# Kernel tuning notes

Hardware: AMD Instinct MI355X
Metric: run time of the kernel (lower is better)

## Reference

```python
import jax, jax.numpy as jnp
import numpy as np

N, E, B, H, L = 100000, 200000, 2048, 256, 4
EPS_MSG = 1e-7   # GENConv message eps
LN_EPS = 1e-5    # torch LayerNorm default eps
SM_EPS = 1e-16   # PyG softmax denominator eps


def layer_norm(x, g, b):
    mu = x.mean(-1, keepdims=True)
    var = ((x - mu) ** 2).mean(-1, keepdims=True)
    return (x - mu) * jax.lax.rsqrt(var + LN_EPS) * g + b


def gen_conv(x, src, dst, eattr, t, W1, b1, lg, lb, W2, b2):
    # GENConv(aggr='softmax', learn_t, num_layers=2, norm='layer')
    msg = jax.nn.relu(x[src] + eattr) + EPS_MSG                      # [E,H]
    scaled = msg * t
    seg_max = jax.ops.segment_max(scaled, dst, num_segments=N)       # [N,H]
    seg_max = jnp.where(jnp.isfinite(seg_max), seg_max, 0.0)
    ex = jnp.exp(scaled - seg_max[dst])                              # [E,H]
    denom = jax.ops.segment_sum(ex, dst, num_segments=N)             # [N,H]
    alpha = ex / (denom[dst] + SM_EPS)
    out = jax.ops.segment_sum(msg * alpha, dst, num_segments=N)      # [N,H]
    out = out + x                                                    # root residual inside GENConv
    h = jax.nn.relu(layer_norm(out @ W1 + b1, lg, lb))               # MLP: Lin -> LN -> ReLU -> Lin
    return h @ W2 + b2


def setup_inputs() -> dict:
    key = jax.random.key(0)
    ks = iter(jax.random.split(key, 16))
    s = lambda *sh: jax.random.normal(next(ks), sh, jnp.float32) * 0.05
    return dict(
        x=jax.random.normal(next(ks), (N, 9), jnp.float32),
        edge_index=jax.random.randint(next(ks), (2, E), 0, N),
        edge_attr=jax.random.normal(next(ks), (E, 3), jnp.float32),
        batch=jnp.sort(jax.random.randint(next(ks), (N,), 0, B)),
        node_W=s(9, H), node_b=jnp.zeros((H,), jnp.float32),
        edge_W=s(3, H), edge_b=jnp.zeros((H,), jnp.float32),
        vn_emb=jnp.zeros((1, H), jnp.float32),
        ln_g=jnp.ones((L, H), jnp.float32), ln_b=jnp.zeros((L, H), jnp.float32),
        t=jnp.ones((L - 1,), jnp.float32),
        mlp_W1=s(L - 1, H, 2 * H), mlp_b1=jnp.zeros((L - 1, 2 * H), jnp.float32),
        mlp_ln_g=jnp.ones((L - 1, 2 * H), jnp.float32), mlp_ln_b=jnp.zeros((L - 1, 2 * H), jnp.float32),
        mlp_W2=s(L - 1, 2 * H, H), mlp_b2=jnp.zeros((L - 1, H), jnp.float32),
    )


def reference(x, edge_index, edge_attr, batch, node_W, node_b, edge_W, edge_b,
              vn_emb, ln_g, ln_b, t, mlp_W1, mlp_b1, mlp_ln_g, mlp_ln_b, mlp_W2, mlp_b2):
    src, dst = edge_index[0], edge_index[1]
    h = x @ node_W + node_b                                          # node encoder
    ea = edge_attr @ edge_W + edge_b                                 # edge encoder
    vn = jnp.broadcast_to(vn_emb, (B, H))
    counts = jax.ops.segment_sum(jnp.ones((N,), h.dtype), batch, num_segments=B)
    inv_counts = (1.0 / jnp.maximum(counts, 1.0))[:, None]           # [B,1]
    # layers[1:] run conv (block='res+'); layers[0] supplies only the final norm+act
    for l in range(1, L):
        hn = jax.nn.relu(layer_norm(h, ln_g[l], ln_b[l]))            # dropout=0.1 is a no-op in eval
        h = h + gen_conv(hn, src, dst, ea, t[l - 1],
                         mlp_W1[l - 1], mlp_b1[l - 1], mlp_ln_g[l - 1], mlp_ln_b[l - 1],
                         mlp_W2[l - 1], mlp_b2[l - 1])
        vn = vn + jax.ops.segment_sum(h, batch, num_segments=B) * inv_counts  # scatter_mean
        h = h + vn[batch]                                            # broadcast virtual node
    h = jax.nn.relu(layer_norm(h, ln_g[0], ln_b[0]))
    return jax.ops.segment_sum(h, batch, num_segments=B) * inv_counts  # global_mean_pool [B,H]
```

## Files before the change

### kernel.cpp

```cpp
#include <hip/hip_runtime.h>
#include <cstdint>
#include <cstddef>


typedef _Float16 half8_t __attribute__((ext_vector_type(8)));
typedef _Float16 half4_t __attribute__((ext_vector_type(4)));
typedef float    floatx4 __attribute__((ext_vector_type(4)));

#define DEVINL __device__ __forceinline__

DEVINL float wave_sum(float v) {
#pragma unroll
  for (int m = 32; m; m >>= 1) v += __shfl_xor(v, m, 64);
  return v;
}

__global__ __launch_bounds__(256) void k_node_enc(
    const float* __restrict__ x, const float* __restrict__ W,
    const float* __restrict__ bias, _Float16* __restrict__ h, int Nr) {
  __shared__ float sW[9 * 256];
  __shared__ float sb[256];
  __shared__ float sx[72];
  const int j = threadIdx.x;
#pragma unroll
  for (int k = 0; k < 9; ++k) sW[k * 256 + j] = W[k * 256 + j];
  sb[j] = bias[j];
  const int row0 = blockIdx.x * 8;
  if (j < 72) {
    int p = row0 * 9 + j;
    sx[j] = (p < Nr * 9) ? x[p] : 0.f;
  }
  __syncthreads();
  for (int r = 0; r < 8; ++r) {
    int row = row0 + r;
    if (row >= Nr) break;
    float acc = sb[j];
#pragma unroll
    for (int k = 0; k < 9; ++k) acc = fmaf(sx[r * 9 + k], sW[k * 256 + j], acc);
    h[(size_t)row * 256 + j] = (_Float16)acc;
  }
}

__global__ void k_bptr(const int* __restrict__ batch, int* __restrict__ bptr,
                       int N_, int B_) {
  int b = blockIdx.x * 256 + threadIdx.x;
  if (b > B_) return;
  int lo = 0, hi = N_;
  while (lo < hi) {
    int mid = (lo + hi) >> 1;
    if (batch[mid] < b) lo = mid + 1; else hi = mid;
  }
  bptr[b] = lo;
}

__global__ void k_deg(const int* __restrict__ ei, int* __restrict__ deg, int E_) {
  int e = blockIdx.x * 256 + threadIdx.x;
  if (e < E_) atomicAdd(&deg[ei[E_ + e]], 1);
}

__global__ __launch_bounds__(256) void k_scan1(
    const int* __restrict__ in, int* __restrict__ out1, int* __restrict__ bsum, int n) {
  __shared__ int tmp[256];
  const int t = threadIdx.x;
  const int base = blockIdx.x * 1024;
  int v[4];
  int run = 0;
#pragma unroll
  for (int i = 0; i < 4; ++i) {
    int p = base + t * 4 + i;
    int xv = (p < n) ? in[p] : 0;
    run += xv;
    v[i] = run;
  }
  tmp[t] = run;
  __syncthreads();
  for (int off = 1; off < 256; off <<= 1) {
    int u = (t >= off) ? tmp[t - off] : 0;
    __syncthreads();
    tmp[t] += u;
    __syncthreads();
  }
  int excl = tmp[t] - run;
#pragma unroll
  for (int i = 0; i < 4; ++i) {
    int p = base + t * 4 + i;
    if (p < n) out1[p] = v[i] + excl;
  }
  if (t == 255) bsum[blockIdx.x] = tmp[255];
}

__global__ void k_scan2(int* bsum, int nb, int* ptr0) {
  if (threadIdx.x == 0 && blockIdx.x == 0) {
    int run = 0;
    for (int i = 0; i < nb; ++i) { int xv = bsum[i]; bsum[i] = run; run += xv; }
    ptr0[0] = 0;
  }
}

__global__ __launch_bounds__(256) void k_scan3(int* out1, const int* __restrict__ bsum, int n) {
  int add = bsum[blockIdx.x];
  int p0 = blockIdx.x * 1024 + threadIdx.x * 4;
#pragma unroll
  for (int i = 0; i < 4; ++i) {
    int p = p0 + i;
    if (p < n) out1[p] += add;
  }
}

__global__ void k_copy(const int* __restrict__ a, int* __restrict__ b, int n) {
  int i = blockIdx.x * 256 + threadIdx.x;
  if (i < n) b[i] = a[i];
}

__global__ void k_csrfill(const int* __restrict__ ei, int* __restrict__ cursor,
                          int* __restrict__ csr_src, int* __restrict__ csr_eid, int E_) {
  int e = blockIdx.x * 256 + threadIdx.x;
  if (e < E_) {
    int d = ei[E_ + e];
    int pos = atomicAdd(&cursor[d], 1);
    csr_src[pos] = ei[e];
    csr_eid[pos] = e;
  }
}

__global__ void k_vninit(const float* __restrict__ emb, float* __restrict__ vn) {
  vn[(size_t)blockIdx.x * 256 + threadIdx.x] = emb[threadIdx.x];
}

__global__ __launch_bounds__(256) void k_wcvt_all(
    const float* __restrict__ W1, const float* __restrict__ W2,
    _Float16* __restrict__ W1T, _Float16* __restrict__ W2T) {
  int idx = blockIdx.x * 256 + threadIdx.x;
  int mat = idx >> 17;
  int rem = idx & 131071;
  if (mat < 3) {
    int k = rem >> 9, n = rem & 511;
    W1T[(size_t)mat * 131072 + (size_t)n * 256 + k] =
        (_Float16)W1[(size_t)mat * 131072 + rem];
  } else {
    int m = mat - 3;
    int k = rem >> 8, n = rem & 255;
    W2T[(size_t)m * 131072 + (size_t)n * 512 + k] =
        (_Float16)W2[(size_t)m * 131072 + rem];
  }
}

__global__ __launch_bounds__(256) void k_ln256(
    const _Float16* __restrict__ h, const float* __restrict__ g,
    const float* __restrict__ b, _Float16* __restrict__ out, int Nr) {
  int row = blockIdx.x * 4 + (threadIdx.x >> 6);
  if (row >= Nr) return;
  int lane = threadIdx.x & 63;
  half4_t xh = *(const half4_t*)(h + (size_t)row * 256 + lane * 4);
  float x0 = (float)xh[0], x1 = (float)xh[1], x2 = (float)xh[2], x3 = (float)xh[3];
  float s = wave_sum(x0 + x1 + x2 + x3);
  float mu = s * (1.f / 256.f);
  float d0 = x0 - mu, d1 = x1 - mu, d2 = x2 - mu, d3 = x3 - mu;
  float v = wave_sum(d0 * d0 + d1 * d1 + d2 * d2 + d3 * d3);
  float rstd = rsqrtf(v * (1.f / 256.f) + 1e-5f);
  float4 gv = *(const float4*)(g + lane * 4);
  float4 bv = *(const float4*)(b + lane * 4);
  half4_t o;
  o[0] = (_Float16)fmaxf(d0 * rstd * gv.x + bv.x, 0.f);
  o[1] = (_Float16)fmaxf(d1 * rstd * gv.y + bv.y, 0.f);
  o[2] = (_Float16)fmaxf(d2 * rstd * gv.z + bv.z, 0.f);
  o[3] = (_Float16)fmaxf(d3 * rstd * gv.w + bv.w, 0.f);
  *(half4_t*)(out + (size_t)row * 256 + lane * 4) = o;
}

__global__ __launch_bounds__(256) void k_aggregate(
    const _Float16* __restrict__ hn, const float* __restrict__ eattr,
    const float* __restrict__ edgeW, const float* __restrict__ edgeB,
    const int* __restrict__ indptr, const int* __restrict__ csr_src,
    const int* __restrict__ csr_eid, const float* __restrict__ tptr,
    _Float16* __restrict__ agg, int Nr) {
  int node = blockIdx.x * 4 + (threadIdx.x >> 6);
  if (node >= Nr) return;
  int lane = threadIdx.x & 63;
  int j0 = lane * 4;
  float4 w0 = *(const float4*)(edgeW + j0);
  float4 w1 = *(const float4*)(edgeW + 256 + j0);
  float4 w2 = *(const float4*)(edgeW + 512 + j0);
  float4 wb = *(const float4*)(edgeB + j0);
  float W0[4] = {w0.x, w0.y, w0.z, w0.w};
  float W1r[4] = {w1.x, w1.y, w1.z, w1.w};
  float W2r[4] = {w2.x, w2.y, w2.z, w2.w};
  float WB[4] = {wb.x, wb.y, wb.z, wb.w};
  float tval = tptr[0];
  int e0 = indptr[node], e1 = indptr[node + 1];
  float D[4] = {0.f, 0.f, 0.f, 0.f};
  float Nu[4] = {0.f, 0.f, 0.f, 0.f};
  for (int s = e0; s < e1; ++s) {
    int srcn = csr_src[s];
    int eid = csr_eid[s];
    float ex0 = eattr[(size_t)eid * 3 + 0];
    float ex1 = eattr[(size_t)eid * 3 + 1];
    float ex2 = eattr[(size_t)eid * 3 + 2];
    half4_t hv = *(const half4_t*)(hn + (size_t)srcn * 256 + j0);
#pragma unroll
    for (int i = 0; i < 4; ++i) {
      float eaj = fmaf(ex0, W0[i], fmaf(ex1, W1r[i], fmaf(ex2, W2r[i], WB[i])));
      float msg = fmaxf((float)hv[i] + eaj, 0.f) + 1e-7f;
      float pr = __expf(msg * tval);
      D[i] += pr;
      Nu[i] = fmaf(pr, msg, Nu[i]);
    }
  }
  half4_t hs = *(const half4_t*)(hn + (size_t)node * 256 + j0);
  half4_t res;
#pragma unroll
  for (int i = 0; i < 4; ++i)
    res[i] = (_Float16)(Nu[i] / (D[i] + 1e-16f) + (float)hs[i]);
  *(half4_t*)(agg + (size_t)node * 256 + j0) = res;
}

__global__ __launch_bounds__(256, 3) void k_gemm1(
    const _Float16* __restrict__ A, const _Float16* __restrict__ BT,
    const float* __restrict__ bias, _Float16* __restrict__ outh,
    float2* __restrict__ rstat, int M) {
  __shared__ _Float16 ldsA[64 * 256];
  __shared__ _Float16 ldsB[128 * 64];
  const int tid = threadIdx.x;
  const int lane = tid & 63;
  const int wv = tid >> 6;
  const int m0 = blockIdx.x * 64;
  const int wm = wv * 16;
  const int q = lane >> 4;
  const int l16 = lane & 15;

  {
    half8_t tmp[8];
    int ss[8];
#pragma unroll
    for (int g = 0; g < 8; ++g) {
      int s = g * 256 + tid;
      int r = s >> 5;
      int c = (s & 31) ^ (r & 7);
      int rowA = m0 + r;
      rowA = rowA < M ? rowA : (M - 1);
      tmp[g] = *(const half8_t*)(A + (size_t)rowA * 256 + c * 8);
      ss[g] = s;
    }
#pragma unroll
    for (int g = 0; g < 8; ++g)
      *(half8_t*)(ldsA + (size_t)ss[g] * 8) = tmp[g];
  }

  size_t offB[4];
  int ldsOffB[4];
#pragma unroll
  for (int i = 0; i < 4; ++i) {
    int p = (i * 4 + wv) * 64 + lane;
    int r = p >> 3;
    int s = p & 7;
    int gg = s ^ (r & 7);
    offB[i] = (size_t)r * 256 + gg * 8;
    ldsOffB[i] = p * 8;
  }
  half8_t rb[4];
  auto loadB = [&](int j) {
    int n = j >> 2, t = j & 3;
    size_t base = (size_t)n * 128 * 256 + t * 64;
#pragma unroll
    for (int i = 0; i < 4; ++i)
      rb[i] = *(const half8_t*)(BT + base + offB[i]);
  };
  auto writeB = [&]() {
#pragma unroll
    for (int i = 0; i < 4; ++i)
      *(half8_t*)(ldsB + ldsOffB[i]) = rb[i];
  };

  floatx4 acc[8] = {};
  float sA[4] = {0.f, 0.f, 0.f, 0.f}, s2A[4] = {0.f, 0.f, 0.f, 0.f};

  loadB(0);
  writeB();
  for (int j = 0; j < 16; ++j) {
    __syncthreads();
    if (j + 1 < 16) loadB(j + 1);
    const int t = j & 3;
#pragma unroll
    for (int kk = 0; kk < 2; ++kk) {
      const int c8 = kk * 4 + q;
      const int cg = t * 8 + c8;
      int r = wm + l16;
      half8_t af = *(const half8_t*)(ldsA + (size_t)(r * 32 + (cg ^ (r & 7))) * 8);
      half8_t bf[8];
#pragma unroll
      for (int ct = 0; ct < 8; ++ct) {
        int n = ct * 16 + l16;
        bf[ct] = *(const half8_t*)(ldsB + (size_t)(n * 8 + (c8 ^ (n & 7))) * 8);
      }
#pragma unroll
      for (int ct = 0; ct < 8; ++ct)
        acc[ct] = __builtin_amdgcn_mfma_f32_16x16x32_f16(af, bf[ct], acc[ct], 0, 0, 0);
    }
    __syncthreads();
    if (j + 1 < 16) writeB();
    if ((j & 3) == 3) {
      int n = j >> 2;
#pragma unroll
      for (int rr = 0; rr < 4; ++rr) {
        int row = m0 + wm + q * 4 + rr;
        float vv[8];
        float s = 0.f, s2 = 0.f;
#pragma unroll
        for (int ct = 0; ct < 8; ++ct) {
          int col = n * 128 + ct * 16 + l16;
          float v = acc[ct][rr] + bias[col];
          vv[ct] = v;
          s += v;
          s2 += v * v;
        }
        if (row < M) {
#pragma unroll
          for (int ct = 0; ct < 8; ++ct) {
            int col = n * 128 + ct * 16 + l16;
            outh[(size_t)row * 512 + col] = (_Float16)vv[ct];
          }
        }
        sA[rr] += s;
        s2A[rr] += s2;
      }
#pragma unroll
      for (int ct = 0; ct < 8; ++ct)
        acc[ct] = floatx4{0.f, 0.f, 0.f, 0.f};
    }
  }

#pragma unroll
  for (int rr = 0; rr < 4; ++rr) {
    float s = sA[rr], s2 = s2A[rr];
#pragma unroll
    for (int m = 1; m < 16; m <<= 1) {
      s += __shfl_xor(s, m, 64);
      s2 += __shfl_xor(s2, m, 64);
    }
    int row = m0 + wm + q * 4 + rr;
    if (l16 == 0 && row < M) rstat[row] = make_float2(s, s2);
  }
}

template <int VN>
__global__ __launch_bounds__(256, 2) void k_gemm2(
    const _Float16* __restrict__ A, const _Float16* __restrict__ BT,
    const float* __restrict__ bias, const float2* __restrict__ rstat,
    const float* __restrict__ lg, const float* __restrict__ lb,
    const float* __restrict__ vn, const int* __restrict__ batch,
    _Float16* __restrict__ outf, int M) {
  constexpr int K = 512, NN = 256, NT = K / 64;
  constexpr int EPS = 68;
  const int g = blockIdx.x;
  const int mI = blockIdx.y * 8 + (g & 7);
  const int nI = g >> 3;
  const int mT = (M + 127) >> 7;
  if (mI >= mT) return;

  __shared__ _Float16 ldsbuf[4 * 64 * EPS];
  _Float16* ldsA = ldsbuf;
  _Float16* ldsB = ldsbuf + 128 * 64;
  __shared__ float sg[512];
  __shared__ float sbt[512];
  const int tid = threadIdx.x;
  sg[tid] = lg[tid];
  sg[tid + 256] = lg[tid + 256];
  sbt[tid] = lb[tid];
  sbt[tid + 256] = lb[tid + 256];
  __syncthreads();

  const int lane = tid & 63;
  const int wv = tid >> 6;
  const int m0 = mI * 128;
  const int n0 = nI * 128;
  const int wm = (wv >> 1) * 64;
  const int wn = (wv & 1) * 64;
  const int q = lane >> 4;
  const int l16 = lane & 15;
  floatx4 acc[4][4] = {};

  size_t offA[4], offB[4];
  int ldsOff[4], gcolA[4];
  float aco[4], cco[4];
#pragma unroll
  for (int i = 0; i < 4; ++i) {
    int p = (i * 4 + wv) * 64 + lane;
    int r = p >> 3;
    int s = p & 7;
    int gg = s ^ (r & 7);
    int rowA = m0 + r;
    rowA = rowA < M ? rowA : (M - 1);
    offA[i] = (size_t)rowA * K + gg * 8;
    offB[i] = (size_t)(n0 + r) * K + gg * 8;
    ldsOff[i] = p * 8;
    gcolA[i] = gg * 8;
    float2 st = rstat[rowA];
    float mu = st.x * (1.f / 512.f);
    float var = st.y * (1.f / 512.f) - mu * mu;
    float rs = rsqrtf(var + 1e-5f);
    aco[i] = rs;
    cco[i] = -mu * rs;
  }
  half8_t ra[4], rb[4];
  auto loadtile = [&](int kt) {
#pragma unroll
    for (int i = 0; i < 4; ++i) {
      ra[i] = *(const half8_t*)(A + offA[i] + kt);
      rb[i] = *(const half8_t*)(BT + offB[i] + kt);
    }
  };
  auto writetile = [&](int kt) {
#pragma unroll
    for (int i = 0; i < 4; ++i) {
      int c0 = kt + gcolA[i];
      half8_t ya;
#pragma unroll
      for (int jj = 0; jj < 8; ++jj) {
        float e = fmaf((float)ra[i][jj], aco[i], cco[i]);
        float y = fmaf(e, sg[c0 + jj], sbt[c0 + jj]);
        ya[jj] = (_Float16)fmaxf(y, 0.f);
      }
      *(half8_t*)(ldsA + ldsOff[i]) = ya;
      *(half8_t*)(ldsB + ldsOff[i]) = rb[i];
    }
  };

  loadtile(0);
  writetile(0);
#pragma unroll
  for (int t = 0; t < NT; ++t) {
    __syncthreads();
    if (t + 1 < NT) loadtile((t + 1) * 64);
#pragma unroll
    for (int kk = 0; kk < 2; ++kk) {
      half8_t af[4], bf[4];
      const int c8 = kk * 4 + q;
#pragma unroll
      for (int rt = 0; rt < 4; ++rt) {
        int r = wm + rt * 16 + l16;
        af[rt] = *(const half8_t*)(ldsA + (size_t)(r * 8 + (c8 ^ (r & 7))) * 8);
      }
#pragma unroll
      for (int ct = 0; ct < 4; ++ct) {
        int n = wn + ct * 16 + l16;
        bf[ct] = *(const half8_t*)(ldsB + (size_t)(n * 8 + (c8 ^ (n & 7))) * 8);
      }
#pragma unroll
      for (int rt = 0; rt < 4; ++rt)
#pragma unroll
        for (int ct = 0; ct < 4; ++ct)
          acc[rt][ct] = __builtin_amdgcn_mfma_f32_16x16x32_f16(af[rt], bf[ct], acc[rt][ct], 0, 0, 0);
    }
    __syncthreads();
    if (t + 1 < NT) writetile((t + 1) * 64);
  }

  _Float16* epi = ldsbuf + wv * (64 * EPS);
#pragma unroll
  for (int rt = 0; rt < 4; ++rt) {
#pragma unroll
    for (int rr = 0; rr < 4; ++rr) {
      int rloc = rt * 16 + q * 4 + rr;
      int row = m0 + wm + rloc;
      int rowc = row < M ? row : (M - 1);
      int bb = 0;
      if constexpr (VN) bb = batch[rowc];
#pragma unroll
      for (int ct = 0; ct < 4; ++ct) {
        int cloc = ct * 16 + l16;
        int col = n0 + wn + cloc;
        float v = acc[rt][ct][rr] + bias[col];
        if constexpr (VN) v += vn[(size_t)bb * 256 + col];
        epi[rloc * EPS + cloc] = (_Float16)v;
      }
    }
  }
#pragma unroll
  for (int it = 0; it < 8; ++it) {
    int rloc = it * 8 + (lane >> 3);
    int row = m0 + wm + rloc;
    if (row < M) {
      int c0 = (lane & 7) * 8;
      size_t gidx = (size_t)row * NN + n0 + wn + c0;
      half8_t hv = *(const half8_t*)(outf + gidx);
      half8_t ev = *(const half8_t*)(epi + rloc * EPS + c0);
      half8_t o;
#pragma unroll
      for (int jj = 0; jj < 8; ++jj) o[jj] = (_Float16)((float)hv[jj] + (float)ev[jj]);
      *(half8_t*)(outf + gidx) = o;
    }
  }
}

__global__ __launch_bounds__(256) void k_vnln(
    const _Float16* __restrict__ h, float* __restrict__ vn,
    const int* __restrict__ bptr, const float* __restrict__ g,
    const float* __restrict__ b, _Float16* __restrict__ hn) {
  __shared__ float red[3][256];
  __shared__ float svn[256];
  int bb = blockIdx.x;
  int w = threadIdx.x >> 6;
  int lane = threadIdx.x & 63;
  int n0 = bptr[bb], n1 = bptr[bb + 1];
  float a0 = 0.f, a1 = 0.f, a2 = 0.f, a3 = 0.f;
  for (int row = n0 + w; row < n1; row += 4) {
    half4_t xh = *(const half4_t*)(h + (size_t)row * 256 + lane * 4);
    a0 += (float)xh[0]; a1 += (float)xh[1];
    a2 += (float)xh[2]; a3 += (float)xh[3];
  }
  if (w > 0) {
    red[w - 1][lane * 4 + 0] = a0;
    red[w - 1][lane * 4 + 1] = a1;
    red[w - 1][lane * 4 + 2] = a2;
    red[w - 1][lane * 4 + 3] = a3;
  }
  __syncthreads();
  if (w == 0) {
    int c = n1 - n0;
    float ic = 1.f / (float)(c > 1 ? c : 1);
#pragma unroll
    for (int k = 0; k < 3; ++k) {
      a0 += red[k][lane * 4 + 0];
      a1 += red[k][lane * 4 + 1];
      a2 += red[k][lane * 4 + 2];
      a3 += red[k][lane * 4 + 3];
    }
    float4 vo = *(const float4*)(vn + (size_t)bb * 256 + lane * 4);
    vo.x += a0 * ic; vo.y += a1 * ic; vo.z += a2 * ic; vo.w += a3 * ic;
    *(float4*)(vn + (size_t)bb * 256 + lane * 4) = vo;
    svn[lane * 4 + 0] = vo.x;
    svn[lane * 4 + 1] = vo.y;
    svn[lane * 4 + 2] = vo.z;
    svn[lane * 4 + 3] = vo.w;
  }
  __syncthreads();
  float4 vv = *(const float4*)(svn + lane * 4);
  float4 gv = *(const float4*)(g + lane * 4);
  float4 bv = *(const float4*)(b + lane * 4);
  for (int row = n0 + w; row < n1; row += 4) {
    half4_t xh = *(const half4_t*)(h + (size_t)row * 256 + lane * 4);
    float x0 = (float)xh[0] + vv.x, x1 = (float)xh[1] + vv.y;
    float x2 = (float)xh[2] + vv.z, x3 = (float)xh[3] + vv.w;
    float s = wave_sum(x0 + x1 + x2 + x3);
    float mu = s * (1.f / 256.f);
    float d0 = x0 - mu, d1 = x1 - mu, d2 = x2 - mu, d3 = x3 - mu;
    float v = wave_sum(d0 * d0 + d1 * d1 + d2 * d2 + d3 * d3);
    float rstd = rsqrtf(v * (1.f / 256.f) + 1e-5f);
    half4_t o;
    o[0] = (_Float16)fmaxf(d0 * rstd * gv.x + bv.x, 0.f);
    o[1] = (_Float16)fmaxf(d1 * rstd * gv.y + bv.y, 0.f);
    o[2] = (_Float16)fmaxf(d2 * rstd * gv.z + bv.z, 0.f);
    o[3] = (_Float16)fmaxf(d3 * rstd * gv.w + bv.w, 0.f);
    *(half4_t*)(hn + (size_t)row * 256 + lane * 4) = o;
  }
}

__global__ __launch_bounds__(256) void k_vnlnpool(
    const _Float16* __restrict__ h, const float* __restrict__ vn,
    const int* __restrict__ bptr, const float* __restrict__ g,
    const float* __restrict__ b, float* __restrict__ out) {
  __shared__ float red[3][256];
  __shared__ float svn[256];
  int bb = blockIdx.x;
  int w = threadIdx.x >> 6;
  int lane = threadIdx.x & 63;
  int n0 = bptr[bb], n1 = bptr[bb + 1];
  int c = n1 - n0;
  float ic = 1.f / (float)(c > 1 ? c : 1);
  float a0 = 0.f, a1 = 0.f, a2 = 0.f, a3 = 0.f;
  for (int row = n0 + w; row < n1; row += 4) {
    half4_t xh = *(const half4_t*)(h + (size_t)row * 256 + lane * 4);
    a0 += (float)xh[0]; a1 += (float)xh[1];
    a2 += (float)xh[2]; a3 += (float)xh[3];
  }
  if (w > 0) {
    red[w - 1][lane * 4 + 0] = a0;
    red[w - 1][lane * 4 + 1] = a1;
    red[w - 1][lane * 4 + 2] = a2;
    red[w - 1][lane * 4 + 3] = a3;
  }
  __syncthreads();
  if (w == 0) {
#pragma unroll
    for (int k = 0; k < 3; ++k) {
      a0 += red[k][lane * 4 + 0];
      a1 += red[k][lane * 4 + 1];
      a2 += red[k][lane * 4 + 2];
      a3 += red[k][lane * 4 + 3];
    }
    float4 vo = *(const float4*)(vn + (size_t)bb * 256 + lane * 4);
    svn[lane * 4 + 0] = vo.x + a0 * ic;
    svn[lane * 4 + 1] = vo.y + a1 * ic;
    svn[lane * 4 + 2] = vo.z + a2 * ic;
    svn[lane * 4 + 3] = vo.w + a3 * ic;
  }
  __syncthreads();
  float4 vv = *(const float4*)(svn + lane * 4);
  float4 gv = *(const float4*)(g + lane * 4);
  float4 bv = *(const float4*)(b + lane * 4);
  a0 = a1 = a2 = a3 = 0.f;
  for (int row = n0 + w; row < n1; row += 4) {
    half4_t xh = *(const half4_t*)(h + (size_t)row * 256 + lane * 4);
    float x0 = (float)xh[0] + vv.x, x1 = (float)xh[1] + vv.y;
    float x2 = (float)xh[2] + vv.z, x3 = (float)xh[3] + vv.w;
    float s = wave_sum(x0 + x1 + x2 + x3);
    float mu = s * (1.f / 256.f);
    float d0 = x0 - mu, d1 = x1 - mu, d2 = x2 - mu, d3 = x3 - mu;
    float v = wave_sum(d0 * d0 + d1 * d1 + d2 * d2 + d3 * d3);
    float rstd = rsqrtf(v * (1.f / 256.f) + 1e-5f);
    a0 += fmaxf(d0 * rstd * gv.x + bv.x, 0.f);
    a1 += fmaxf(d1 * rstd * gv.y + bv.y, 0.f);
    a2 += fmaxf(d2 * rstd * gv.z + bv.z, 0.f);
    a3 += fmaxf(d3 * rstd * gv.w + bv.w, 0.f);
  }
  __syncthreads();
  if (w > 0) {
    red[w - 1][lane * 4 + 0] = a0;
    red[w - 1][lane * 4 + 1] = a1;
    red[w - 1][lane * 4 + 2] = a2;
    red[w - 1][lane * 4 + 3] = a3;
  }
  __syncthreads();
  if (w == 0) {
#pragma unroll
    for (int k = 0; k < 3; ++k) {
      a0 += red[k][lane * 4 + 0];
      a1 += red[k][lane * 4 + 1];
      a2 += red[k][lane * 4 + 2];
      a3 += red[k][lane * 4 + 3];
    }
    float4 o = {a0 * ic, a1 * ic, a2 * ic, a3 * ic};
    *(float4*)(out + (size_t)bb * 256 + lane * 4) = o;
  }
}

extern "C" void kernel_launch(void* const* d_in, const int* in_sizes, int n_in,
                              void* d_out, int out_size, void* d_ws, size_t ws_size,
                              hipStream_t stream) {
  const float* x      = (const float*)d_in[0];
  const int*   ei     = (const int*)d_in[1];
  const float* eattr  = (const float*)d_in[2];
  const int*   batch  = (const int*)d_in[3];
  const float* nodeW  = (const float*)d_in[4];
  const float* nodeB  = (const float*)d_in[5];
  const float* edgeW  = (const float*)d_in[6];
  const float* edgeB  = (const float*)d_in[7];
  const float* vnemb  = (const float*)d_in[8];
  const float* lng    = (const float*)d_in[9];
  const float* lnb    = (const float*)d_in[10];
  const float* tparam = (const float*)d_in[11];
  const float* W1     = (const float*)d_in[12];
  const float* b1     = (const float*)d_in[13];
  const float* mlng   = (const float*)d_in[14];
  const float* mlnb   = (const float*)d_in[15];
  const float* W2     = (const float*)d_in[16];
  const float* b2     = (const float*)d_in[17];
  float* out = (float*)d_out;

  const int N = in_sizes[3];
  const int E = in_sizes[1] / 2;
  const int B = out_size / 256;

  char* p = (char*)d_ws;
  auto take = [&](size_t bytes) -> char* {
    char* r = p;
    p += (bytes + 255) & ~(size_t)255;
    return r;
  };
  _Float16*  h   = (_Float16*)take((size_t)N * 256 * 2);
  _Float16*  t1  = (_Float16*)take((size_t)N * 512 * 2);
  _Float16*  hn  = t1;
  _Float16*  agg = (_Float16*)take((size_t)N * 256 * 2);
  _Float16*  W1T = (_Float16*)take((size_t)3 * 512 * 256 * 2);
  _Float16*  W2T = (_Float16*)take((size_t)3 * 256 * 512 * 2);
  float2*    rstat = (float2*)take((size_t)N * 8);
  float*     vn  = (float*)take((size_t)B * 256 * 4);
  int*       bptr   = (int*)take((size_t)(B + 1) * 4);
  int*       deg    = (int*)take((size_t)N * 4);
  int*       indptr = (int*)take((size_t)(N + 1) * 4);
  int*       cursor = (int*)take((size_t)N * 4);
  int*       csr_src = (int*)take((size_t)E * 4);
  int*       csr_eid = (int*)take((size_t)E * 4);
  int*       bsum    = (int*)take(512 * 4);
  (void)ws_size; (void)n_in;

  hipMemsetAsync(deg, 0, (size_t)N * 4, stream);

  k_node_enc<<<(N + 7) / 8, 256, 0, stream>>>(x, nodeW, nodeB, h, N);
  k_bptr<<<(B + 256) / 256, 256, 0, stream>>>(batch, bptr, N, B);

  const int nbN = (N + 1023) / 1024;
  k_deg<<<(E + 255) / 256, 256, 0, stream>>>(ei, deg, E);
  k_scan1<<<nbN, 256, 0, stream>>>(deg, indptr + 1, bsum, N);
  k_scan2<<<1, 64, 0, stream>>>(bsum, nbN, indptr);
  k_scan3<<<nbN, 256, 0, stream>>>(indptr + 1, bsum, N);
  k_copy<<<(N + 255) / 256, 256, 0, stream>>>(indptr, cursor, N);
  k_csrfill<<<(E + 255) / 256, 256, 0, stream>>>(ei, cursor, csr_src, csr_eid, E);

  k_wcvt_all<<<3072, 256, 0, stream>>>(W1, W2, W1T, W2T);
  k_vninit<<<B, 256, 0, stream>>>(vnemb, vn);

  const int lnGrid = (N + 3) / 4;
  const int mTiles1 = (N + 63) / 64;
  const int mTiles2 = (N + 127) / 128;
  const dim3 g2grid(16, (mTiles2 + 7) / 8);

  k_ln256<<<lnGrid, 256, 0, stream>>>(h, lng + 256, lnb + 256, hn, N);
  for (int l = 1; l <= 3; ++l) {
    k_aggregate<<<lnGrid, 256, 0, stream>>>(hn, eattr, edgeW, edgeB, indptr, csr_src, csr_eid,
                                            tparam + (l - 1), agg, N);
    k_gemm1<<<mTiles1, 256, 0, stream>>>(
        agg, W1T + (size_t)(l - 1) * 512 * 256, b1 + (size_t)(l - 1) * 512, t1, rstat, N);
    if (l == 1)
      k_gemm2<0><<<g2grid, 256, 0, stream>>>(
          t1, W2T + (size_t)(l - 1) * 256 * 512, b2 + (size_t)(l - 1) * 256, rstat,
          mlng + (size_t)(l - 1) * 512, mlnb + (size_t)(l - 1) * 512, nullptr, nullptr, h, N);
    else
      k_gemm2<1><<<g2grid, 256, 0, stream>>>(
          t1, W2T + (size_t)(l - 1) * 256 * 512, b2 + (size_t)(l - 1) * 256, rstat,
          mlng + (size_t)(l - 1) * 512, mlnb + (size_t)(l - 1) * 512, vn, batch, h, N);
    if (l < 3)
      k_vnln<<<B, 256, 0, stream>>>(h, vn, bptr,
                                    lng + (size_t)(l + 1) * 256, lnb + (size_t)(l + 1) * 256, hn);
    else
      k_vnlnpool<<<B, 256, 0, stream>>>(h, vn, bptr, lng, lnb, out);
  }
}
```

Baseline: 767.7 us.

## Stage gemm1 epilogue through LDS for vector stores; fuse cursor copy into scan

The gemm1 epilogue previously wrote each fp16 output element with a scalar strided store. It now writes the tile to a padded per-wave LDS buffer and re-reads it as 8-half vectors, giving coalesced 16-byte global stores. The k_copy kernel is removed because k_scan3 now writes the cursor array directly, saving one launch and one pass over memory. The extra LDS drops gemm1's launch bound from 3 to 2 blocks per CU, which may cut occupancy.

```diff
diff --git a/kernel.cpp b/kernel.cpp
--- a/kernel.cpp
+++ b/kernel.cpp
@@ -97,19 +97,20 @@
   }
 }
 
-__global__ __launch_bounds__(256) void k_scan3(int* out1, const int* __restrict__ bsum, int n) {
+__global__ __launch_bounds__(256) void k_scan3(
+    int* out1, const int* __restrict__ bsum, int* __restrict__ cursor, int n) {
   int add = bsum[blockIdx.x];
   int p0 = blockIdx.x * 1024 + threadIdx.x * 4;
 #pragma unroll
   for (int i = 0; i < 4; ++i) {
     int p = p0 + i;
-    if (p < n) out1[p] += add;
-  }
-}
-
-__global__ void k_copy(const int* __restrict__ a, int* __restrict__ b, int n) {
-  int i = blockIdx.x * 256 + threadIdx.x;
-  if (i < n) b[i] = a[i];
+    if (p < n) {
+      int v = out1[p] + add;
+      out1[p] = v;
+      cursor[p + 1] = v;
+    }
+  }
+  if (blockIdx.x == 0 && threadIdx.x == 0) cursor[0] = 0;
 }
 
 __global__ void k_csrfill(const int* __restrict__ ei, int* __restrict__ cursor,
@@ -214,12 +215,14 @@
   *(half4_t*)(agg + (size_t)node * 256 + j0) = res;
 }
 
-__global__ __launch_bounds__(256, 3) void k_gemm1(
+__global__ __launch_bounds__(256, 2) void k_gemm1(
     const _Float16* __restrict__ A, const _Float16* __restrict__ BT,
     const float* __restrict__ bias, _Float16* __restrict__ outh,
     float2* __restrict__ rstat, int M) {
+  constexpr int EPS = 132;
   __shared__ _Float16 ldsA[64 * 256];
   __shared__ _Float16 ldsB[128 * 64];
+  __shared__ _Float16 ldsE[4 * 16 * EPS];
   const int tid = threadIdx.x;
   const int lane = tid & 63;
   const int wv = tid >> 6;
@@ -227,6 +230,7 @@
   const int wm = wv * 16;
   const int q = lane >> 4;
   const int l16 = lane & 15;
+  _Float16* epi = ldsE + wv * (16 * EPS);
 
   {
     half8_t tmp[8];
@@ -302,26 +306,27 @@
       int n = j >> 2;
 #pragma unroll
       for (int rr = 0; rr < 4; ++rr) {
-        int row = m0 + wm + q * 4 + rr;
-        float vv[8];
+        int rloc = q * 4 + rr;
         float s = 0.f, s2 = 0.f;
 #pragma unroll
         for (int ct = 0; ct < 8; ++ct) {
           int col = n * 128 + ct * 16 + l16;
           float v = acc[ct][rr] + bias[col];
-          vv[ct] = v;
+          epi[rloc * EPS + ct * 16 + l16] = (_Float16)v;
           s += v;
           s2 += v * v;
         }
-        if (row < M) {
-#pragma unroll
-          for (int ct = 0; ct < 8; ++ct) {
-            int col = n * 128 + ct * 16 + l16;
-            outh[(size_t)row * 512 + col] = (_Float16)vv[ct];
-          }
-        }
         sA[rr] += s;
         s2A[rr] += s2;
+      }
+#pragma unroll
+      for (int it = 0; it < 4; ++it) {
+        int rloc = it * 4 + q;
+        int row = m0 + wm + rloc;
+        if (row < M) {
+          half8_t ev = *(const half8_t*)(epi + rloc * EPS + l16 * 8);
+          *(half8_t*)(outh + (size_t)row * 512 + n * 128 + l16 * 8) = ev;
+        }
       }
 #pragma unroll
       for (int ct = 0; ct < 8; ++ct)
@@ -678,7 +683,7 @@
   int*       bptr   = (int*)take((size_t)(B + 1) * 4);
   int*       deg    = (int*)take((size_t)N * 4);
   int*       indptr = (int*)take((size_t)(N + 1) * 4);
-  int*       cursor = (int*)take((size_t)N * 4);
+  int*       cursor = (int*)take((size_t)(N + 1) * 4);
   int*       csr_src = (int*)take((size_t)E * 4);
   int*       csr_eid = (int*)take((size_t)E * 4);
   int*       bsum    = (int*)take(512 * 4);
@@ -693,8 +698,7 @@
   k_deg<<<(E + 255) / 256, 256, 0, stream>>>(ei, deg, E);
   k_scan1<<<nbN, 256, 0, stream>>>(deg, indptr + 1, bsum, N);
   k_scan2<<<1, 64, 0, stream>>>(bsum, nbN, indptr);
-  k_scan3<<<nbN, 256, 0, stream>>>(indptr + 1, bsum, N);
-  k_copy<<<(N + 255) / 256, 256, 0, stream>>>(indptr, cursor, N);
+  k_scan3<<<nbN, 256, 0, stream>>>(indptr + 1, bsum, cursor, N);
   k_csrfill<<<(E + 255) / 256, 256, 0, stream>>>(ei, cursor, csr_src, csr_eid, E);
 
   k_wcvt_all<<<3072, 256, 0, stream>>>(W1, W2, W1T, W2T);
```

Result: slower. 823.7 us (+7.3%).
